# Performance work log

Measured on AMD Instinct MI355X. Metric: run time of the kernel, lower is better.

## Reference

```python
import jax, jax.numpy as jnp
import numpy as np

N_HEAD = 12


def setup_inputs() -> dict:
    key = jax.random.key(0)
    ks = jax.random.split(key, 16)
    B, N, D, P, H = 1, 512, 384, 128, N_HEAD
    s = 0.02
    return {
        'x1d': jax.random.normal(ks[0], (B, N, D), jnp.float32),
        'x2d': jax.random.normal(ks[1], (B, N, N, P), jnp.float32),
        'pose_t': jax.random.normal(ks[2], (B, N, 3), jnp.float32),
        'pose_r': jax.random.normal(ks[3], (B, N, 3, 3), jnp.float32),
        'bias': jnp.zeros((B, 1, N, N), jnp.float32),
        'w_sq': jax.random.normal(ks[4], (D, D), jnp.float32) * s,
        'w_sk': jax.random.normal(ks[5], (D, D), jnp.float32) * s,
        'w_sv': jax.random.normal(ks[6], (D, D), jnp.float32) * s,
        'w_pb': jax.random.normal(ks[7], (P, H), jnp.float32) * s,
        'w_pq': jax.random.normal(ks[8], (D, H * 3 * 4), jnp.float32) * s,
        'w_pk': jax.random.normal(ks[9], (D, H * 3 * 4), jnp.float32) * s,
        'w_pv': jax.random.normal(ks[10], (D, H * 3 * 8), jnp.float32) * s,
        'tpw': jax.random.uniform(ks[11], (H,), jnp.float32),
        'w_pairv': jax.random.normal(ks[12], (P, D), jnp.float32) * s,
        'w_out': jax.random.normal(ks[13], (2 * D + H * 8 * 4, D), jnp.float32) * s,
        'b_out': jnp.zeros((D,), jnp.float32),
    }


def reference(x1d, x2d, pose_t, pose_r, bias, w_sq, w_sk, w_sv, w_pb,
              w_pq, w_pk, w_pv, tpw, w_pairv, w_out, b_out):
    B, N, D = x1d.shape
    H = N_HEAD
    dk = D // H
    scalar_w = 1.0 / np.sqrt(3 * dk)
    point_w_c = 1.0 / np.sqrt(3 * 4 * 9 / 2)
    pair_w = 1.0 / np.sqrt(3)

    T = pose_t                                # [B,N,3]
    R = jnp.swapaxes(pose_r, -1, -2)          # [B,N,3,3] (pose[1]^T as in torch code)

    # scalar attention
    q_s = (x1d @ w_sq).reshape(B, N, H, dk)
    k_s = (x1d @ w_sk).reshape(B, N, H, dk)
    v_s = (x1d @ w_sv).reshape(B, N, H, dk)
    scalar_attn = jnp.einsum('bihc,bjhc->bhij', q_s * scalar_w, k_s)

    # point attention (global frame)
    def affine(pt):  # R @ pt + T
        return jnp.einsum('bnxy,bnhpy->bnhpx', R, pt) + T[:, :, None, None, :]

    q_p = affine((x1d @ w_pq).reshape(B, N, H, 4, 3))
    k_p = affine((x1d @ w_pk).reshape(B, N, H, 4, 3))
    v_p = affine((x1d @ w_pv).reshape(B, N, H, 8, 3))

    dist = jnp.linalg.norm(q_p[:, :, None] - k_p[:, None], axis=-1)  # [B,I,J,H,P]
    pw = point_w_c * jax.nn.softplus(tpw)                            # [H]
    point_attn = -0.5 * pw[:, None, None] * jnp.transpose(dist.sum(-1), (0, 3, 1, 2))

    # pair bias attention
    pair_attn = pair_w * jnp.transpose(x2d @ w_pb, (0, 3, 1, 2))     # [B,H,I,J]

    attn = jax.nn.softmax(scalar_attn + point_attn + pair_attn + bias, axis=-1)

    # aggregations
    out_scalar = jnp.einsum('bhij,bjhc->bihc', attn, v_s).reshape(B, N, D)

    out_pg = jnp.einsum('bhij,bjhcp->bihcp', attn, v_p)              # [B,I,H,8,3]
    # inverse affine: R^T @ (x - T)
    out_pl = jnp.einsum('bnyx,bnhpy->bnhpx', R, out_pg - T[:, :, None, None, :])
    out_pn = jnp.linalg.norm(out_pl, axis=-1).reshape(B, N, H * 8)
    out_pl = out_pl.reshape(B, N, H * 8 * 3)

    v_pair = (x2d @ w_pairv).reshape(B, N, N, H, dk)
    out_pair = jnp.einsum('bhij,bijhc->bihc', attn, v_pair).reshape(B, N, D)

    feat = jnp.concatenate([out_scalar, out_pl, out_pair, out_pn], axis=-1)
    return feat @ w_out + b_out
```

## Files before the change

### kernel.cpp

```cpp
#include <hip/hip_runtime.h>
#include <hip/hip_bf16.h>
#include <math.h>

#define N_  512
#define D_  384
#define H_  12
#define DK_ 32
#define P_  128

typedef short short8 __attribute__((ext_vector_type(8)));
typedef float f32x4  __attribute__((ext_vector_type(4)));

static __device__ __forceinline__ unsigned short f2bf(float f) {
    union { float f; unsigned int u; } v; v.f = f;
    unsigned int r = (v.u + 0x7FFFu + ((v.u >> 16) & 1u)) >> 16;
    return (unsigned short)r;
}
static __device__ __forceinline__ float bf2f(unsigned short u) {
    union { unsigned int u; float f; } v; v.u = ((unsigned int)u) << 16;
    return v.f;
}
static __device__ __forceinline__ short2 pk2bf(float a, float b) {
    __hip_bfloat162 h = __float22bfloat162_rn(make_float2(a, b));
    return *(short2*)&h;
}
typedef union { short8 v; short2 h2[4]; } s8u;

__global__ __launch_bounds__(384) void k_front(
    const float* __restrict__ x2d, const float* __restrict__ w_pb,
    float* __restrict__ pairlog,
    const float* __restrict__ x1d, const float* __restrict__ pose_t,
    const float* __restrict__ pose_r,
    const float* __restrict__ w_sq, const float* __restrict__ w_sk,
    const float* __restrict__ w_sv, const float* __restrict__ w_pq,
    const float* __restrict__ w_pk, const float* __restrict__ w_pv,
    float* __restrict__ qs, float* __restrict__ kst,
    float* __restrict__ qp, float* __restrict__ kpt,
    unsigned short* __restrict__ vcatT)
{
    __shared__ float raw[8][288];
    __shared__ float Rsh[8][9];
    __shared__ float Tsh[8][3];

    const int t = threadIdx.x;

    if (blockIdx.x < 2048) {
        if (t >= 256) return;
        const int wid  = t >> 6;
        const int lane = t & 63;
        const int quad = lane >> 4;
        const int col  = lane & 15;
        const float pair_w = 0.57735027f;

        short8 bfr[4];
        #pragma unroll
        for (int kt = 0; kt < 4; ++kt) {
            #pragma unroll
            for (int jj = 0; jj < 8; ++jj) {
                int p = kt * 32 + quad * 8 + jj;
                bfr[kt][jj] = (col < 12) ? (short)f2bf(w_pb[p * 12 + col]) : (short)0;
            }
        }
        #pragma unroll
        for (int s = 0; s < 2; ++s) {
            const int T  = blockIdx.x * 8 + wid * 2 + s;
            const int i  = T >> 5;
            const int j0 = (T & 31) << 4;
            const float* xrow = x2d + ((size_t)(i * N_) + j0 + col) * P_;

            f32x4 acc = {0.f, 0.f, 0.f, 0.f};
            #pragma unroll
            for (int kt = 0; kt < 4; ++kt) {
                const int k0 = kt * 32 + quad * 8;
                float4 f0 = *(const float4*)(xrow + k0);
                float4 f1 = *(const float4*)(xrow + k0 + 4);
                s8u afr;
                afr.h2[0] = pk2bf(f0.x, f0.y);
                afr.h2[1] = pk2bf(f0.z, f0.w);
                afr.h2[2] = pk2bf(f1.x, f1.y);
                afr.h2[3] = pk2bf(f1.z, f1.w);
                acc = __builtin_amdgcn_mfma_f32_16x16x32_bf16(afr.v, bfr[kt], acc, 0, 0, 0);
            }
            if (col < 12) {
                #pragma unroll
                for (int r = 0; r < 4; ++r) {
                    int j = j0 + quad * 4 + r;
                    pairlog[((size_t)(col * N_ + i)) * N_ + j] = pair_w * acc[r];
                }
            }
        }
        return;
    }

    const int b   = blockIdx.x - 2048;
    const int seg = b >> 6;
    const int i0  = (b & 63) * 8;

    if (seg < 3) {
        const float* __restrict__ w = (seg == 0) ? w_sq : (seg == 1) ? w_sk : w_sv;
        float acc[8];
        #pragma unroll
        for (int r = 0; r < 8; ++r) acc[r] = 0.f;
        for (int d = 0; d < D_; d += 4) {
            float4 xr[8];
            #pragma unroll
            for (int r = 0; r < 8; ++r)
                xr[r] = *(const float4*)(x1d + (i0 + r) * D_ + d);
            #pragma unroll
            for (int e = 0; e < 4; ++e) {
                float wv = w[(d + e) * D_ + t];
                #pragma unroll
                for (int r = 0; r < 8; ++r)
                    acc[r] += ((const float*)&xr[r])[e] * wv;
            }
        }
        if (seg == 0) {
            #pragma unroll
            for (int r = 0; r < 8; ++r) qs[(i0 + r) * D_ + t] = acc[r];
        } else if (seg == 1) {
            *(float4*)(kst + t * N_ + i0)     = make_float4(acc[0], acc[1], acc[2], acc[3]);
            *(float4*)(kst + t * N_ + i0 + 4) = make_float4(acc[4], acc[5], acc[6], acc[7]);
        } else {
            int h = t >> 5, c = t & 31;
            s8u sv;
            #pragma unroll
            for (int r = 0; r < 4; ++r) sv.h2[r] = pk2bf(acc[2*r], acc[2*r+1]);
            *(short8*)(vcatT + ((size_t)h * 64 + c) * N_ + i0) = sv.v;
        }
    } else {
        if (t < 72) Rsh[t / 9][t % 9] = pose_r[(i0 + t / 9) * 9 + t % 9];
        else if (t < 96) {
            int r = (t - 72) / 3, c = (t - 72) % 3;
            Tsh[r][c] = pose_t[(i0 + r) * 3 + c];
        }

        if (t < 288) {
            const float* __restrict__ w;
            int col, ldw;
            if (seg == 3) {
                if (t < 144) { w = w_pq; col = t;       ldw = 144; }
                else         { w = w_pk; col = t - 144; ldw = 144; }
            } else         { w = w_pv; col = t;       ldw = 288; }
            float acc[8];
            #pragma unroll
            for (int r = 0; r < 8; ++r) acc[r] = 0.f;
            for (int d = 0; d < D_; d += 4) {
                float4 xr[8];
                #pragma unroll
                for (int r = 0; r < 8; ++r)
                    xr[r] = *(const float4*)(x1d + (i0 + r) * D_ + d);
                #pragma unroll
                for (int e = 0; e < 4; ++e) {
                    float wv = w[(d + e) * ldw + col];
                    #pragma unroll
                    for (int r = 0; r < 8; ++r)
                        acc[r] += ((const float*)&xr[r])[e] * wv;
                }
            }
            #pragma unroll
            for (int r = 0; r < 8; ++r) raw[r][t] = acc[r];
        }
        __syncthreads();

        if (t < 288) {
            const int x3   = t % 3;
            const int base = t - x3;
            if (seg == 3) {
                const int c = (t < 144) ? t : t - 144;
                if (t < 144) {
                    #pragma unroll
                    for (int r = 0; r < 8; ++r) {
                        float g = Rsh[r][0 + x3] * raw[r][base]
                                + Rsh[r][3 + x3] * raw[r][base + 1]
                                + Rsh[r][6 + x3] * raw[r][base + 2] + Tsh[r][x3];
                        qp[(i0 + r) * 144 + c] = g;
                    }
                } else {
                    float g[8];
                    #pragma unroll
                    for (int r = 0; r < 8; ++r)
                        g[r] = Rsh[r][0 + x3] * raw[r][base]
                             + Rsh[r][3 + x3] * raw[r][base + 1]
                             + Rsh[r][6 + x3] * raw[r][base + 2] + Tsh[r][x3];
                    *(float4*)(kpt + c * N_ + i0)     = make_float4(g[0], g[1], g[2], g[3]);
                    *(float4*)(kpt + c * N_ + i0 + 4) = make_float4(g[4], g[5], g[6], g[7]);
                }
            } else {
                int h = t / 24, pc = t % 24;
                float g[8];
                #pragma unroll
                for (int r = 0; r < 8; ++r)
                    g[r] = Rsh[r][0 + x3] * raw[r][base]
                         + Rsh[r][3 + x3] * raw[r][base + 1]
                         + Rsh[r][6 + x3] * raw[r][base + 2] + Tsh[r][x3];
                s8u sv;
                #pragma unroll
                for (int r = 0; r < 4; ++r) sv.h2[r] = pk2bf(g[2*r], g[2*r+1]);
                *(short8*)(vcatT + ((size_t)h * 64 + 32 + pc) * N_ + i0) = sv.v;
            }
        }
    }
}

__global__ __launch_bounds__(256) void k_sp_soft(
    const float* __restrict__ qs, const float* __restrict__ kst,
    const float* __restrict__ qp, const float* __restrict__ kpt,
    const float* __restrict__ bias, const float* __restrict__ tpw,
    const float* __restrict__ pairlog,
    unsigned short* __restrict__ attn_bf)
{
    const int h  = blockIdx.x / 128;
    const int i0 = (blockIdx.x % 128) * 4;
    const int t  = threadIdx.x;
    const int lane = t & 63;
    const int wid  = t >> 6;
    __shared__ float qsh[4][32];
    __shared__ float qph[4][12];
    __shared__ float wredm[4][4];
    __shared__ float wreds[4][4];
    if (t < 128) { int il = t / 32, c = t % 32; qsh[il][c] = qs[(i0+il) * D_ + h*32 + c]; }
    else if (t < 176) { int r = t - 128; int il = r / 12, c = r % 12; qph[il][c] = qp[(i0+il)*144 + h*12 + c]; }
    const float pwh = 0.13608276f * log1pf(expf(tpw[h]));
    const float scalar_w = 0.10206207f;
    __syncthreads();

    float v[4][2];
    for (int jh = 0; jh < 2; ++jh) {
        int j = t + jh * 256;
        float kv[32];
        #pragma unroll
        for (int c = 0; c < 32; ++c) kv[c] = kst[(h*32 + c) * N_ + j];
        float kp[12];
        #pragma unroll
        for (int c = 0; c < 12; ++c) kp[c] = kpt[(h*12 + c) * N_ + j];

        #pragma unroll
        for (int il = 0; il < 4; ++il) {
            float s = 0.f;
            #pragma unroll
            for (int c = 0; c < 32; ++c) s += qsh[il][c] * kv[c];
            float dsum = 0.f;
            #pragma unroll
            for (int p = 0; p < 4; ++p) {
                float dx = qph[il][p*3+0] - kp[p*3+0];
                float dy = qph[il][p*3+1] - kp[p*3+1];
                float dz = qph[il][p*3+2] - kp[p*3+2];
                dsum += sqrtf(dx*dx + dy*dy + dz*dz);
            }
            v[il][jh] = scalar_w * s - 0.5f * pwh * dsum
                      + bias[(i0+il) * N_ + j]
                      + pairlog[((size_t)(h * N_ + (i0+il))) * N_ + j];
        }
    }

    #pragma unroll
    for (int il = 0; il < 4; ++il) {
        float mt = fmaxf(v[il][0], v[il][1]);
        #pragma unroll
        for (int off = 1; off < 64; off <<= 1)
            mt = fmaxf(mt, __shfl_xor(mt, off));
        if (lane == 0) wredm[il][wid] = mt;
    }
    __syncthreads();
    float m[4];
    #pragma unroll
    for (int il = 0; il < 4; ++il)
        m[il] = fmaxf(fmaxf(wredm[il][0], wredm[il][1]),
                      fmaxf(wredm[il][2], wredm[il][3]));

    #pragma unroll
    for (int il = 0; il < 4; ++il) {
        float e0 = __expf(v[il][0] - m[il]);
        float e1 = __expf(v[il][1] - m[il]);
        v[il][0] = e0; v[il][1] = e1;
        float st = e0 + e1;
        #pragma unroll
        for (int off = 1; off < 64; off <<= 1)
            st += __shfl_xor(st, off);
        if (lane == 0) wreds[il][wid] = st;
    }
    __syncthreads();
    #pragma unroll
    for (int il = 0; il < 4; ++il) {
        float inv = 1.0f / (wreds[il][0] + wreds[il][1] + wreds[il][2] + wreds[il][3]);
        size_t base = ((size_t)(h * N_ + i0 + il)) * N_;
        attn_bf[base + t]       = f2bf(v[il][0] * inv);
        attn_bf[base + t + 256] = f2bf(v[il][1] * inv);
    }
}

__global__ __launch_bounds__(256) void k_mid(
    const unsigned short* __restrict__ attn_bf,
    const float* __restrict__ x2d,
    const unsigned short* __restrict__ vcatT,
    float* __restrict__ tmp,
    float* __restrict__ feat, float* __restrict__ outpg)
{
    __shared__ float4 at[3][N_];
    __shared__ float red[4][1536];

    const int t = threadIdx.x;

    if (blockIdx.x < 512) {
        const int i = blockIdx.x;
        for (int idx = t; idx < 12 * N_; idx += 256) {
            int h = idx >> 9, j = idx & 511;
            float a = bf2f(attn_bf[((size_t)(h * N_ + i)) * N_ + j]);
            ((float*)&at[h >> 2][j])[h & 3] = a;
        }
        __syncthreads();

        const int p2 = (t & 63) * 2;
        const int jh = t >> 6;
        float acc[12][2];
        #pragma unroll
        for (int h = 0; h < 12; ++h) { acc[h][0] = 0.f; acc[h][1] = 0.f; }
        const float* xb = x2d + (size_t)i * N_ * P_;

        #pragma unroll 4
        for (int j = jh; j < N_; j += 4) {
            float2 x = *(const float2*)(xb + j * P_ + p2);
            float4 a0 = at[0][j], a1 = at[1][j], a2 = at[2][j];
            acc[0][0]  += a0.x*x.x; acc[0][1]  += a0.x*x.y;
            acc[1][0]  += a0.y*x.x; acc[1][1]  += a0.y*x.y;
            acc[2][0]  += a0.z*x.x; acc[2][1]  += a0.z*x.y;
            acc[3][0]  += a0.w*x.x; acc[3][1]  += a0.w*x.y;
            acc[4][0]  += a1.x*x.x; acc[4][1]  += a1.x*x.y;
            acc[5][0]  += a1.y*x.x; acc[5][1]  += a1.y*x.y;
            acc[6][0]  += a1.z*x.x; acc[6][1]  += a1.z*x.y;
            acc[7][0]  += a1.w*x.x; acc[7][1]  += a1.w*x.y;
            acc[8][0]  += a2.x*x.x; acc[8][1]  += a2.x*x.y;
            acc[9][0]  += a2.y*x.x; acc[9][1]  += a2.y*x.y;
            acc[10][0] += a2.z*x.x; acc[10][1] += a2.z*x.y;
            acc[11][0] += a2.w*x.x; acc[11][1] += a2.w*x.y;
        }
        #pragma unroll
        for (int h = 0; h < 12; ++h) {
            red[jh][h * 128 + p2]     = acc[h][0];
            red[jh][h * 128 + p2 + 1] = acc[h][1];
        }
        __syncthreads();
        for (int idx = t; idx < 1536; idx += 256)
            tmp[(size_t)i * 1536 + idx] = red[0][idx] + red[1][idx] + red[2][idx] + red[3][idx];
        return;
    }

    const int bid  = blockIdx.x - 512;
    const int h    = bid >> 5;
    const int i0   = (bid & 31) << 4;
    const int wid  = t >> 6;
    const int lane = t & 63;
    const int quad = lane >> 4;
    const int col  = lane & 15;
    const int c    = wid * 16 + col;
    const bool cvalid = (c < 56);

    const unsigned short* arow = attn_bf + ((size_t)(h * N_ + i0 + col)) * N_;
    const unsigned short* brow = vcatT + ((size_t)h * 64 + c) * N_;

    f32x4 acc = {0.f, 0.f, 0.f, 0.f};
    #pragma unroll
    for (int kt = 0; kt < 16; ++kt) {
        const int k0 = kt * 32 + quad * 8;
        short8 a = *(const short8*)(arow + k0);
        short8 b;
        if (cvalid) b = *(const short8*)(brow + k0);
        else { b[0]=0;b[1]=0;b[2]=0;b[3]=0;b[4]=0;b[5]=0;b[6]=0;b[7]=0; }
        acc = __builtin_amdgcn_mfma_f32_16x16x32_bf16(a, b, acc, 0, 0, 0);
    }
    #pragma unroll
    for (int r = 0; r < 4; ++r) {
        int i = i0 + quad * 4 + r;
        if (c < 32)       feat[(size_t)i * 1152 + h * 32 + c] = acc[r];
        else if (c < 56)  outpg[((size_t)i * 12 + h) * 24 + (c - 32)] = acc[r];
    }
}

__global__ __launch_bounds__(384) void k_feat(
    const float* __restrict__ tmp, const float* __restrict__ outpg,
    const float* __restrict__ pose_t, const float* __restrict__ pose_r,
    const float* __restrict__ w_pairv, float* __restrict__ feat)
{
    const int i = blockIdx.x;
    const int t = threadIdx.x;
    __shared__ float tsh[1536];
    __shared__ float pg[288];
    __shared__ float pl[288];
    __shared__ float Rsh[9], Tsh[3];

    for (int idx = t; idx < 1536; idx += 384) tsh[idx] = tmp[(size_t)i * 1536 + idx];
    if (t < 288) pg[t] = outpg[i * 288 + t];
    if (t < 9) Rsh[t] = pose_r[i * 9 + t];
    if (t < 3) Tsh[t] = pose_t[i * 3 + t];
    __syncthreads();

    {
        int h = t >> 5;
        const float* ts = tsh + h * 128;
        float acc = 0.f;
        #pragma unroll 4
        for (int p = 0; p < 128; ++p) acc += ts[p] * w_pairv[p * D_ + t];
        feat[(size_t)i * 1152 + 672 + t] = acc;
    }
    if (t < 288) {
        int x3 = t % 3, base = t - x3;
        float g0 = pg[base + 0] - Tsh[0];
        float g1 = pg[base + 1] - Tsh[1];
        float g2 = pg[base + 2] - Tsh[2];
        float v = Rsh[x3*3+0]*g0 + Rsh[x3*3+1]*g1 + Rsh[x3*3+2]*g2;
        pl[t] = v;
        feat[(size_t)i * 1152 + 384 + t] = v;
    }
    __syncthreads();
    if (t < 96) {
        float a = pl[t*3], b = pl[t*3+1], c = pl[t*3+2];
        feat[(size_t)i * 1152 + 1056 + t] = sqrtf(a*a + b*b + c*c);
    }
}

__global__ __launch_bounds__(384) void k_out_part(
    const float* __restrict__ feat, const float* __restrict__ w_out,
    float* __restrict__ part)
{
    const int kc = blockIdx.x >> 6;
    const int i0 = (blockIdx.x & 63) * 8;
    const int t  = threadIdx.x;
    const int k0 = kc * 144;

    float acc[8];
    #pragma unroll
    for (int r = 0; r < 8; ++r) acc[r] = 0.f;

    for (int d = 0; d < 144; d += 4) {
        float4 fr[8];
        #pragma unroll
        for (int r = 0; r < 8; ++r)
            fr[r] = *(const float4*)(feat + (size_t)(i0 + r) * 1152 + k0 + d);
        #pragma unroll
        for (int e = 0; e < 4; ++e) {
            float wv = w_out[(size_t)(k0 + d + e) * D_ + t];
            #pragma unroll
            for (int r = 0; r < 8; ++r)
                acc[r] += ((const float*)&fr[r])[e] * wv;
        }
    }
    #pragma unroll
    for (int r = 0; r < 8; ++r)
        part[((size_t)kc * N_ + i0 + r) * D_ + t] = acc[r];
}

__global__ __launch_bounds__(256) void k_out_red(
    const float* __restrict__ part, const float* __restrict__ b_out,
    float* __restrict__ out)
{
    const int idx = blockIdx.x * 256 + threadIdx.x;
    float s = b_out[idx % D_];
    #pragma unroll
    for (int kc = 0; kc < 8; ++kc) s += part[(size_t)kc * (N_ * D_) + idx];
    out[idx] = s;
}

extern "C" void kernel_launch(void* const* d_in, const int* in_sizes, int n_in,
                              void* d_out, int out_size, void* d_ws, size_t ws_size,
                              hipStream_t stream)
{
    (void)in_sizes; (void)n_in; (void)out_size; (void)ws_size;
    const float* x1d     = (const float*)d_in[0];
    const float* x2d     = (const float*)d_in[1];
    const float* pose_t  = (const float*)d_in[2];
    const float* pose_r  = (const float*)d_in[3];
    const float* bias    = (const float*)d_in[4];
    const float* w_sq    = (const float*)d_in[5];
    const float* w_sk    = (const float*)d_in[6];
    const float* w_sv    = (const float*)d_in[7];
    const float* w_pb    = (const float*)d_in[8];
    const float* w_pq    = (const float*)d_in[9];
    const float* w_pk    = (const float*)d_in[10];
    const float* w_pv    = (const float*)d_in[11];
    const float* tpw     = (const float*)d_in[12];
    const float* w_pairv = (const float*)d_in[13];
    const float* w_out   = (const float*)d_in[14];
    const float* b_out   = (const float*)d_in[15];
    float* out = (float*)d_out;

    float* ws = (float*)d_ws;
    float* qs      = ws;
    float* kst     = qs      + 196608;
    float* qp      = kst     + 196608;
    float* kpt     = qp      + 73728;
    float* pairlog = kpt     + 73728;
    float* tmp     = pairlog + 3145728;
    float* outpg   = tmp     + 786432;
    float* feat    = outpg   + 147456;
    float* part    = feat    + 589824;
    unsigned short* attn_bf = (unsigned short*)(part + 1572864);
    unsigned short* vcatT   = attn_bf + (size_t)12 * N_ * N_;

    hipLaunchKernelGGL(k_front, dim3(2048 + 320), dim3(384), 0, stream,
                       x2d, w_pb, pairlog,
                       x1d, pose_t, pose_r, w_sq, w_sk, w_sv, w_pq, w_pk, w_pv,
                       qs, kst, qp, kpt, vcatT);
    hipLaunchKernelGGL(k_sp_soft, dim3(12 * 128), dim3(256), 0, stream,
                       qs, kst, qp, kpt, bias, tpw, pairlog, attn_bf);
    hipLaunchKernelGGL(k_mid, dim3(512 + 384), dim3(256), 0, stream,
                       attn_bf, x2d, vcatT, tmp, feat, outpg);
    hipLaunchKernelGGL(k_feat, dim3(N_), dim3(384), 0, stream,
                       tmp, outpg, pose_t, pose_r, w_pairv, feat);
    hipLaunchKernelGGL(k_out_part, dim3(512), dim3(384), 0, stream,
                       feat, w_out, part);
    hipLaunchKernelGGL(k_out_red, dim3(768), dim3(256), 0, stream,
                       part, b_out, out);
}
```

Baseline: 361.3 us.

## Use all warps for pair-bias tiles, hoist x2d loads, halve projection rows per block

The pair-bias part of k_front now uses all six waves per block instead of four, so fewer blocks are needed. All x2d loads are issued ahead of the MFMA work behind a sched_barrier to raise memory-level parallelism, and the pairlog stores become float4 writes. The projection blocks now handle 4 rows instead of 8, doubling their block count to spread the small GEMMs across more CUs. The cost is more registers held for the prefetched tiles and extra redundant weight reads in the projection blocks.

Result: slower. 368.9 us (+2.1%).

```diff
diff --git a/kernel.cpp b/kernel.cpp
--- a/kernel.cpp
+++ b/kernel.cpp
@@ -8,6 +8,8 @@
 #define DK_ 32
 #define P_  128
 
+#define NPB 1366
+
 typedef short short8 __attribute__((ext_vector_type(8)));
 typedef float f32x4  __attribute__((ext_vector_type(4)));
 
@@ -25,6 +27,7 @@
     return *(short2*)&h;
 }
 typedef union { short8 v; short2 h2[4]; } s8u;
+typedef union { short2 h2[2]; unsigned long long u; } s4u;
 
 __global__ __launch_bounds__(384) void k_front(
     const float* __restrict__ x2d, const float* __restrict__ w_pb,
@@ -38,14 +41,13 @@
     float* __restrict__ qp, float* __restrict__ kpt,
     unsigned short* __restrict__ vcatT)
 {
-    __shared__ float raw[8][288];
-    __shared__ float Rsh[8][9];
-    __shared__ float Tsh[8][3];
+    __shared__ float raw[4][288];
+    __shared__ float Rsh[4][9];
+    __shared__ float Tsh[4][3];
 
     const int t = threadIdx.x;
 
-    if (blockIdx.x < 2048) {
-        if (t >= 256) return;
+    if (blockIdx.x < NPB) {
         const int wid  = t >> 6;
         const int lane = t & 63;
         const int quad = lane >> 4;
@@ -61,76 +63,91 @@
                 bfr[kt][jj] = (col < 12) ? (short)f2bf(w_pb[p * 12 + col]) : (short)0;
             }
         }
+
+        const int Tb = blockIdx.x * 12 + wid * 2;
+
+        float4 f[2][8];
+        int iA[2], j0A[2];
         #pragma unroll
         for (int s = 0; s < 2; ++s) {
-            const int T  = blockIdx.x * 8 + wid * 2 + s;
-            const int i  = T >> 5;
-            const int j0 = (T & 31) << 4;
-            const float* xrow = x2d + ((size_t)(i * N_) + j0 + col) * P_;
-
-            f32x4 acc = {0.f, 0.f, 0.f, 0.f};
-            #pragma unroll
-            for (int kt = 0; kt < 4; ++kt) {
-                const int k0 = kt * 32 + quad * 8;
-                float4 f0 = *(const float4*)(xrow + k0);
-                float4 f1 = *(const float4*)(xrow + k0 + 4);
-                s8u afr;
-                afr.h2[0] = pk2bf(f0.x, f0.y);
-                afr.h2[1] = pk2bf(f0.z, f0.w);
-                afr.h2[2] = pk2bf(f1.x, f1.y);
-                afr.h2[3] = pk2bf(f1.z, f1.w);
-                acc = __builtin_amdgcn_mfma_f32_16x16x32_bf16(afr.v, bfr[kt], acc, 0, 0, 0);
-            }
-            if (col < 12) {
-                #pragma unroll
-                for (int r = 0; r < 4; ++r) {
-                    int j = j0 + quad * 4 + r;
-                    pairlog[((size_t)(col * N_ + i)) * N_ + j] = pair_w * acc[r];
+            const int T = Tb + s;
+            iA[s]  = T >> 5;
+            j0A[s] = (T & 31) << 4;
+            if (T < 16384) {
+                const float* xrow = x2d + ((size_t)(iA[s] * N_) + j0A[s] + col) * P_;
+                #pragma unroll
+                for (int kt = 0; kt < 4; ++kt) {
+                    f[s][2*kt]   = *(const float4*)(xrow + kt * 32 + quad * 8);
+                    f[s][2*kt+1] = *(const float4*)(xrow + kt * 32 + quad * 8 + 4);
                 }
             }
         }
+        __builtin_amdgcn_sched_barrier(0);
+
+        #pragma unroll
+        for (int s = 0; s < 2; ++s) {
+            const int T = Tb + s;
+            if (T < 16384) {
+                f32x4 acc = {0.f, 0.f, 0.f, 0.f};
+                #pragma unroll
+                for (int kt = 0; kt < 4; ++kt) {
+                    s8u afr;
+                    afr.h2[0] = pk2bf(f[s][2*kt].x,   f[s][2*kt].y);
+                    afr.h2[1] = pk2bf(f[s][2*kt].z,   f[s][2*kt].w);
+                    afr.h2[2] = pk2bf(f[s][2*kt+1].x, f[s][2*kt+1].y);
+                    afr.h2[3] = pk2bf(f[s][2*kt+1].z, f[s][2*kt+1].w);
+                    acc = __builtin_amdgcn_mfma_f32_16x16x32_bf16(afr.v, bfr[kt], acc, 0, 0, 0);
+                }
+                if (col < 12) {
+                    float4 st = make_float4(pair_w * acc[0], pair_w * acc[1],
+                                            pair_w * acc[2], pair_w * acc[3]);
+                    *(float4*)(pairlog + ((size_t)(col * N_ + iA[s])) * N_
+                               + j0A[s] + quad * 4) = st;
+                }
+            }
+        }
         return;
     }
 
-    const int b   = blockIdx.x - 2048;
-    const int seg = b >> 6;
-    const int i0  = (b & 63) * 8;
+    const int b   = blockIdx.x - NPB;
+    const int seg = b >> 7;
+    const int i0  = (b & 127) * 4;
 
     if (seg < 3) {
         const float* __restrict__ w = (seg == 0) ? w_sq : (seg == 1) ? w_sk : w_sv;
-        float acc[8];
-        #pragma unroll
-        for (int r = 0; r < 8; ++r) acc[r] = 0.f;
+        float acc[4];
+        #pragma unroll
+        for (int r = 0; r < 4; ++r) acc[r] = 0.f;
+        #pragma unroll 2
         for (int d = 0; d < D_; d += 4) {
-            float4 xr[8];
-            #pragma unroll
-            for (int r = 0; r < 8; ++r)
+            float4 xr[4];
+            #pragma unroll
+            for (int r = 0; r < 4; ++r)
                 xr[r] = *(const float4*)(x1d + (i0 + r) * D_ + d);
             #pragma unroll
             for (int e = 0; e < 4; ++e) {
                 float wv = w[(d + e) * D_ + t];
                 #pragma unroll
-                for (int r = 0; r < 8; ++r)
+                for (int r = 0; r < 4; ++r)
                     acc[r] += ((const float*)&xr[r])[e] * wv;
             }
         }
         if (seg == 0) {
             #pragma unroll
-            for (int r = 0; r < 8; ++r) qs[(i0 + r) * D_ + t] = acc[r];
+            for (int r = 0; r < 4; ++r) qs[(i0 + r) * D_ + t] = acc[r];
         } else if (seg == 1) {
-            *(float4*)(kst + t * N_ + i0)     = make_float4(acc[0], acc[1], acc[2], acc[3]);
-            *(float4*)(kst + t * N_ + i0 + 4) = make_float4(acc[4], acc[5], acc[6], acc[7]);
+            *(float4*)(kst + t * N_ + i0) = make_float4(acc[0], acc[1], acc[2], acc[3]);
         } else {
             int h = t >> 5, c = t & 31;
-            s8u sv;
-            #pragma unroll
-            for (int r = 0; r < 4; ++r) sv.h2[r] = pk2bf(acc[2*r], acc[2*r+1]);
-            *(short8*)(vcatT + ((size_t)h * 64 + c) * N_ + i0) = sv.v;
+            s4u sv;
+            sv.h2[0] = pk2bf(acc[0], acc[1]);
+            sv.h2[1] = pk2bf(acc[2], acc[3]);
+            *(unsigned long long*)(vcatT + ((size_t)h * 64 + c) * N_ + i0) = sv.u;
         }
     } else {
-        if (t < 72) Rsh[t / 9][t % 9] = pose_r[(i0 + t / 9) * 9 + t % 9];
-        else if (t < 96) {
-            int r = (t - 72) / 3, c = (t - 72) % 3;
+        if (t < 36) Rsh[t / 9][t % 9] = pose_r[(i0 + t / 9) * 9 + t % 9];
+        else if (t < 48) {
+            int r = (t - 36) / 3, c = (t - 36) % 3;
             Tsh[r][c] = pose_t[(i0 + r) * 3 + c];
         }
 
@@ -141,24 +158,25 @@
                 if (t < 144) { w = w_pq; col = t;       ldw = 144; }
                 else         { w = w_pk; col = t - 144; ldw = 144; }
             } else         { w = w_pv; col = t;       ldw = 288; }
-            float acc[8];
-            #pragma unroll
-            for (int r = 0; r < 8; ++r) acc[r] = 0.f;
+            float acc[4];
+            #pragma unroll
+            for (int r = 0; r < 4; ++r) acc[r] = 0.f;
+            #pragma unroll 2
             for (int d = 0; d < D_; d += 4) {
-                float4 xr[8];
-                #pragma unroll
-                for (int r = 0; r < 8; ++r)
+                float4 xr[4];
+                #pragma unroll
+                for (int r = 0; r < 4; ++r)
                     xr[r] = *(const float4*)(x1d + (i0 + r) * D_ + d);
                 #pragma unroll
                 for (int e = 0; e < 4; ++e) {
                     float wv = w[(d + e) * ldw + col];
                     #pragma unroll
-                    for (int r = 0; r < 8; ++r)
+                    for (int r = 0; r < 4; ++r)
                         acc[r] += ((const float*)&xr[r])[e] * wv;
                 }
             }
             #pragma unroll
-            for (int r = 0; r < 8; ++r) raw[r][t] = acc[r];
+            for (int r = 0; r < 4; ++r) raw[r][t] = acc[r];
         }
         __syncthreads();
 
@@ -167,36 +185,31 @@
             const int base = t - x3;
             if (seg == 3) {
                 const int c = (t < 144) ? t : t - 144;
+                float g[4];
+                #pragma unroll
+                for (int r = 0; r < 4; ++r)
+                    g[r] = Rsh[r][0 + x3] * raw[r][base]
+                         + Rsh[r][3 + x3] * raw[r][base + 1]
+                         + Rsh[r][6 + x3] * raw[r][base + 2] + Tsh[r][x3];
                 if (t < 144) {
                     #pragma unroll
-                    for (int r = 0; r < 8; ++r) {
-                        float g = Rsh[r][0 + x3] * raw[r][base]
-                                + Rsh[r][3 + x3] * raw[r][base + 1]
-                                + Rsh[r][6 + x3] * raw[r][base + 2] + Tsh[r][x3];
-                        qp[(i0 + r) * 144 + c] = g;
-                    }
+                    for (int r = 0; r < 4; ++r)
+                        qp[(i0 + r) * 144 + c] = g[r];
                 } else {
-                    float g[8];
-                    #pragma unroll
-                    for (int r = 0; r < 8; ++r)
-                        g[r] = Rsh[r][0 + x3] * raw[r][base]
-                             + Rsh[r][3 + x3] * raw[r][base + 1]
-                             + Rsh[r][6 + x3] * raw[r][base + 2] + Tsh[r][x3];
-                    *(float4*)(kpt + c * N_ + i0)     = make_float4(g[0], g[1], g[2], g[3]);
-                    *(float4*)(kpt + c * N_ + i0 + 4) = make_float4(g[4], g[5], g[6], g[7]);
+                    *(float4*)(kpt + c * N_ + i0) = make_float4(g[0], g[1], g[2], g[3]);
                 }
             } else {
                 int h = t / 24, pc = t % 24;
-                float g[8];
-                #pragma unroll
-                for (int r = 0; r < 8; ++r)
+                float g[4];
+                #pragma unroll
+                for (int r = 0; r < 4; ++r)
                     g[r] = Rsh[r][0 + x3] * raw[r][base]
                          + Rsh[r][3 + x3] * raw[r][base + 1]
                          + Rsh[r][6 + x3] * raw[r][base + 2] + Tsh[r][x3];
-                s8u sv;
-                #pragma unroll
-                for (int r = 0; r < 4; ++r) sv.h2[r] = pk2bf(g[2*r], g[2*r+1]);
-                *(short8*)(vcatT + ((size_t)h * 64 + 32 + pc) * N_ + i0) = sv.v;
+                s4u sv;
+                sv.h2[0] = pk2bf(g[0], g[1]);
+                sv.h2[1] = pk2bf(g[2], g[3]);
+                *(unsigned long long*)(vcatT + ((size_t)h * 64 + 32 + pc) * N_ + i0) = sv.u;
             }
         }
     }
@@ -496,7 +509,7 @@
     unsigned short* attn_bf = (unsigned short*)(part + 1572864);
     unsigned short* vcatT   = attn_bf + (size_t)12 * N_ * N_;
 
-    hipLaunchKernelGGL(k_front, dim3(2048 + 320), dim3(384), 0, stream,
+    hipLaunchKernelGGL(k_front, dim3(NPB + 640), dim3(384), 0, stream,
                        x2d, w_pb, pairlog,
                        x1d, pose_t, pose_r, w_sq, w_sk, w_sv, w_pq, w_pk, w_pv,
                        qs, kst, qp, kpt, vcatT);
```

## Persist pair-bias blocks with double-buffered loads and halve grids of later kernels

Applied to the files above, without the earlier changes.

The pair-bias projection in k_front becomes a persistent-style loop. 512 blocks of 6 waves each process strided tiles, double-buffering the x2d loads so the next tile's loads overlap the current MFMA, and stores use float4. Projection blocks are moved to the front of the grid. The other kernels (softmax, feat, out_part, out_red) each process 2–3 virtual blocks per physical block with smaller grids, which amortizes setup but reduces parallelism and adds extra syncs.

Measured after the change: 388.1 us. 7.4% more time.

```diff
diff --git a/kernel.cpp b/kernel.cpp
--- a/kernel.cpp
+++ b/kernel.cpp
@@ -7,6 +7,9 @@
 #define H_  12
 #define DK_ 32
 #define P_  128
+
+#define PROJ_B 320
+#define PAIR_B 512
 
 typedef short short8 __attribute__((ext_vector_type(8)));
 typedef float f32x4  __attribute__((ext_vector_type(4)));
@@ -44,12 +47,13 @@
 
     const int t = threadIdx.x;
 
-    if (blockIdx.x < 2048) {
-        if (t >= 256) return;
+    if (blockIdx.x >= PROJ_B) {
+        const int pb   = blockIdx.x - PROJ_B;
         const int wid  = t >> 6;
         const int lane = t & 63;
         const int quad = lane >> 4;
         const int col  = lane & 15;
+        const int gw   = pb * 6 + wid;
         const float pair_w = 0.57735027f;
 
         short8 bfr[4];
@@ -61,38 +65,51 @@
                 bfr[kt][jj] = (col < 12) ? (short)f2bf(w_pb[p * 12 + col]) : (short)0;
             }
         }
-        #pragma unroll
-        for (int s = 0; s < 2; ++s) {
-            const int T  = blockIdx.x * 8 + wid * 2 + s;
+
+        auto ldt = [&](float4* f, int T) {
             const int i  = T >> 5;
             const int j0 = (T & 31) << 4;
             const float* xrow = x2d + ((size_t)(i * N_) + j0 + col) * P_;
-
+            #pragma unroll
+            for (int kt = 0; kt < 4; ++kt) {
+                f[2*kt]   = *(const float4*)(xrow + kt * 32 + quad * 8);
+                f[2*kt+1] = *(const float4*)(xrow + kt * 32 + quad * 8 + 4);
+            }
+        };
+        auto cmpt = [&](const float4* f, int T) {
             f32x4 acc = {0.f, 0.f, 0.f, 0.f};
             #pragma unroll
             for (int kt = 0; kt < 4; ++kt) {
-                const int k0 = kt * 32 + quad * 8;
-                float4 f0 = *(const float4*)(xrow + k0);
-                float4 f1 = *(const float4*)(xrow + k0 + 4);
                 s8u afr;
-                afr.h2[0] = pk2bf(f0.x, f0.y);
-                afr.h2[1] = pk2bf(f0.z, f0.w);
-                afr.h2[2] = pk2bf(f1.x, f1.y);
-                afr.h2[3] = pk2bf(f1.z, f1.w);
+                afr.h2[0] = pk2bf(f[2*kt].x,   f[2*kt].y);
+                afr.h2[1] = pk2bf(f[2*kt].z,   f[2*kt].w);
+                afr.h2[2] = pk2bf(f[2*kt+1].x, f[2*kt+1].y);
+                afr.h2[3] = pk2bf(f[2*kt+1].z, f[2*kt+1].w);
                 acc = __builtin_amdgcn_mfma_f32_16x16x32_bf16(afr.v, bfr[kt], acc, 0, 0, 0);
             }
             if (col < 12) {
-                #pragma unroll
-                for (int r = 0; r < 4; ++r) {
-                    int j = j0 + quad * 4 + r;
-                    pairlog[((size_t)(col * N_ + i)) * N_ + j] = pair_w * acc[r];
-                }
-            }
-        }
+                const int i  = T >> 5;
+                const int j0 = (T & 31) << 4;
+                float4 st = make_float4(pair_w * acc[0], pair_w * acc[1],
+                                        pair_w * acc[2], pair_w * acc[3]);
+                *(float4*)(pairlog + ((size_t)(col * N_ + i)) * N_ + j0 + quad * 4) = st;
+            }
+        };
+
+        float4 fA[8], fB[8];
+        const bool has6 = (gw + 15360) < 16384;
+        ldt(fA, gw);
+        ldt(fB, gw + 3072);
+        cmpt(fA, gw);          ldt(fA, gw + 6144);
+        cmpt(fB, gw + 3072);   ldt(fB, gw + 9216);
+        cmpt(fA, gw + 6144);   ldt(fA, gw + 12288);
+        cmpt(fB, gw + 9216);   if (has6) ldt(fB, gw + 15360);
+        cmpt(fA, gw + 12288);
+        if (has6) cmpt(fB, gw + 15360);
         return;
     }
 
-    const int b   = blockIdx.x - 2048;
+    const int b   = blockIdx.x;
     const int seg = b >> 6;
     const int i0  = (b & 63) * 8;
 
@@ -209,83 +226,89 @@
     const float* __restrict__ pairlog,
     unsigned short* __restrict__ attn_bf)
 {
-    const int h  = blockIdx.x / 128;
-    const int i0 = (blockIdx.x % 128) * 4;
-    const int t  = threadIdx.x;
+    const int t = threadIdx.x;
     const int lane = t & 63;
     const int wid  = t >> 6;
     __shared__ float qsh[4][32];
     __shared__ float qph[4][12];
     __shared__ float wredm[4][4];
     __shared__ float wreds[4][4];
-    if (t < 128) { int il = t / 32, c = t % 32; qsh[il][c] = qs[(i0+il) * D_ + h*32 + c]; }
-    else if (t < 176) { int r = t - 128; int il = r / 12, c = r % 12; qph[il][c] = qp[(i0+il)*144 + h*12 + c]; }
-    const float pwh = 0.13608276f * log1pf(expf(tpw[h]));
-    const float scalar_w = 0.10206207f;
-    __syncthreads();
-
-    float v[4][2];
-    for (int jh = 0; jh < 2; ++jh) {
-        int j = t + jh * 256;
-        float kv[32];
-        #pragma unroll
-        for (int c = 0; c < 32; ++c) kv[c] = kst[(h*32 + c) * N_ + j];
-        float kp[12];
-        #pragma unroll
-        for (int c = 0; c < 12; ++c) kp[c] = kpt[(h*12 + c) * N_ + j];
+
+    for (int u = 0; u < 2; ++u) {
+        const int vb = blockIdx.x + u * 768;
+        const int h  = vb / 128;
+        const int i0 = (vb % 128) * 4;
+
+        if (t < 128) { int il = t / 32, c = t % 32; qsh[il][c] = qs[(i0+il) * D_ + h*32 + c]; }
+        else if (t < 176) { int r = t - 128; int il = r / 12, c = r % 12; qph[il][c] = qp[(i0+il)*144 + h*12 + c]; }
+        const float pwh = 0.13608276f * log1pf(expf(tpw[h]));
+        const float scalar_w = 0.10206207f;
+        __syncthreads();
+
+        float v[4][2];
+        for (int jh = 0; jh < 2; ++jh) {
+            int j = t + jh * 256;
+            float kv[32];
+            #pragma unroll
+            for (int c = 0; c < 32; ++c) kv[c] = kst[(h*32 + c) * N_ + j];
+            float kp[12];
+            #pragma unroll
+            for (int c = 0; c < 12; ++c) kp[c] = kpt[(h*12 + c) * N_ + j];
+
+            #pragma unroll
+            for (int il = 0; il < 4; ++il) {
+                float s = 0.f;
+                #pragma unroll
+                for (int c = 0; c < 32; ++c) s += qsh[il][c] * kv[c];
+                float dsum = 0.f;
+                #pragma unroll
+                for (int p = 0; p < 4; ++p) {
+                    float dx = qph[il][p*3+0] - kp[p*3+0];
+                    float dy = qph[il][p*3+1] - kp[p*3+1];
+                    float dz = qph[il][p*3+2] - kp[p*3+2];
+                    dsum += sqrtf(dx*dx + dy*dy + dz*dz);
+                }
+                v[il][jh] = scalar_w * s - 0.5f * pwh * dsum
+                          + bias[(i0+il) * N_ + j]
+                          + pairlog[((size_t)(h * N_ + (i0+il))) * N_ + j];
+            }
+        }
 
         #pragma unroll
         for (int il = 0; il < 4; ++il) {
-            float s = 0.f;
-            #pragma unroll
-            for (int c = 0; c < 32; ++c) s += qsh[il][c] * kv[c];
-            float dsum = 0.f;
-            #pragma unroll
-            for (int p = 0; p < 4; ++p) {
-                float dx = qph[il][p*3+0] - kp[p*3+0];
-                float dy = qph[il][p*3+1] - kp[p*3+1];
-                float dz = qph[il][p*3+2] - kp[p*3+2];
-                dsum += sqrtf(dx*dx + dy*dy + dz*dz);
-            }
-            v[il][jh] = scalar_w * s - 0.5f * pwh * dsum
-                      + bias[(i0+il) * N_ + j]
-                      + pairlog[((size_t)(h * N_ + (i0+il))) * N_ + j];
-        }
-    }
-
-    #pragma unroll
-    for (int il = 0; il < 4; ++il) {
-        float mt = fmaxf(v[il][0], v[il][1]);
-        #pragma unroll
-        for (int off = 1; off < 64; off <<= 1)
-            mt = fmaxf(mt, __shfl_xor(mt, off));
-        if (lane == 0) wredm[il][wid] = mt;
-    }
-    __syncthreads();
-    float m[4];
-    #pragma unroll
-    for (int il = 0; il < 4; ++il)
-        m[il] = fmaxf(fmaxf(wredm[il][0], wredm[il][1]),
-                      fmaxf(wredm[il][2], wredm[il][3]));
-
-    #pragma unroll
-    for (int il = 0; il < 4; ++il) {
-        float e0 = __expf(v[il][0] - m[il]);
-        float e1 = __expf(v[il][1] - m[il]);
-        v[il][0] = e0; v[il][1] = e1;
-        float st = e0 + e1;
-        #pragma unroll
-        for (int off = 1; off < 64; off <<= 1)
-            st += __shfl_xor(st, off);
-        if (lane == 0) wreds[il][wid] = st;
-    }
-    __syncthreads();
-    #pragma unroll
-    for (int il = 0; il < 4; ++il) {
-        float inv = 1.0f / (wreds[il][0] + wreds[il][1] + wreds[il][2] + wreds[il][3]);
-        size_t base = ((size_t)(h * N_ + i0 + il)) * N_;
-        attn_bf[base + t]       = f2bf(v[il][0] * inv);
-        attn_bf[base + t + 256] = f2bf(v[il][1] * inv);
+            float mt = fmaxf(v[il][0], v[il][1]);
+            #pragma unroll
+            for (int off = 1; off < 64; off <<= 1)
+                mt = fmaxf(mt, __shfl_xor(mt, off));
+            if (lane == 0) wredm[il][wid] = mt;
+        }
+        __syncthreads();
+        float m[4];
+        #pragma unroll
+        for (int il = 0; il < 4; ++il)
+            m[il] = fmaxf(fmaxf(wredm[il][0], wredm[il][1]),
+                          fmaxf(wredm[il][2], wredm[il][3]));
+
+        #pragma unroll
+        for (int il = 0; il < 4; ++il) {
+            float e0 = __expf(v[il][0] - m[il]);
+            float e1 = __expf(v[il][1] - m[il]);
+            v[il][0] = e0; v[il][1] = e1;
+            float st = e0 + e1;
+            #pragma unroll
+            for (int off = 1; off < 64; off <<= 1)
+                st += __shfl_xor(st, off);
+            if (lane == 0) wreds[il][wid] = st;
+        }
+        __syncthreads();
+        #pragma unroll
+        for (int il = 0; il < 4; ++il) {
+            float inv = 1.0f / (wreds[il][0] + wreds[il][1] + wreds[il][2] + wreds[il][3]);
+            size_t base = ((size_t)(h * N_ + i0 + il)) * N_;
+            attn_bf[base + t]       = f2bf(v[il][0] * inv);
+            attn_bf[base + t + 256] = f2bf(v[il][1] * inv);
+        }
+        __syncthreads();
     }
 }
 
@@ -381,40 +404,44 @@
     const float* __restrict__ pose_t, const float* __restrict__ pose_r,
     const float* __restrict__ w_pairv, float* __restrict__ feat)
 {
-    const int i = blockIdx.x;
     const int t = threadIdx.x;
     __shared__ float tsh[1536];
     __shared__ float pg[288];
     __shared__ float pl[288];
     __shared__ float Rsh[9], Tsh[3];
 
-    for (int idx = t; idx < 1536; idx += 384) tsh[idx] = tmp[(size_t)i * 1536 + idx];
-    if (t < 288) pg[t] = outpg[i * 288 + t];
-    if (t < 9) Rsh[t] = pose_r[i * 9 + t];
-    if (t < 3) Tsh[t] = pose_t[i * 3 + t];
-    __syncthreads();
-
-    {
-        int h = t >> 5;
-        const float* ts = tsh + h * 128;
-        float acc = 0.f;
-        #pragma unroll 4
-        for (int p = 0; p < 128; ++p) acc += ts[p] * w_pairv[p * D_ + t];
-        feat[(size_t)i * 1152 + 672 + t] = acc;
-    }
-    if (t < 288) {
-        int x3 = t % 3, base = t - x3;
-        float g0 = pg[base + 0] - Tsh[0];
-        float g1 = pg[base + 1] - Tsh[1];
-        float g2 = pg[base + 2] - Tsh[2];
-        float v = Rsh[x3*3+0]*g0 + Rsh[x3*3+1]*g1 + Rsh[x3*3+2]*g2;
-        pl[t] = v;
-        feat[(size_t)i * 1152 + 384 + t] = v;
-    }
-    __syncthreads();
-    if (t < 96) {
-        float a = pl[t*3], b = pl[t*3+1], c = pl[t*3+2];
-        feat[(size_t)i * 1152 + 1056 + t] = sqrtf(a*a + b*b + c*c);
+    for (int u = 0; u < 2; ++u) {
+        const int i = blockIdx.x + u * 256;
+
+        for (int idx = t; idx < 1536; idx += 384) tsh[idx] = tmp[(size_t)i * 1536 + idx];
+        if (t < 288) pg[t] = outpg[i * 288 + t];
+        if (t < 9) Rsh[t] = pose_r[i * 9 + t];
+        if (t < 3) Tsh[t] = pose_t[i * 3 + t];
+        __syncthreads();
+
+        {
+            int h = t >> 5;
+            const float* ts = tsh + h * 128;
+            float acc = 0.f;
+            #pragma unroll 4
+            for (int p = 0; p < 128; ++p) acc += ts[p] * w_pairv[p * D_ + t];
+            feat[(size_t)i * 1152 + 672 + t] = acc;
+        }
+        if (t < 288) {
+            int x3 = t % 3, base = t - x3;
+            float g0 = pg[base + 0] - Tsh[0];
+            float g1 = pg[base + 1] - Tsh[1];
+            float g2 = pg[base + 2] - Tsh[2];
+            float v = Rsh[x3*3+0]*g0 + Rsh[x3*3+1]*g1 + Rsh[x3*3+2]*g2;
+            pl[t] = v;
+            feat[(size_t)i * 1152 + 384 + t] = v;
+        }
+        __syncthreads();
+        if (t < 96) {
+            float a = pl[t*3], b = pl[t*3+1], c = pl[t*3+2];
+            feat[(size_t)i * 1152 + 1056 + t] = sqrtf(a*a + b*b + c*c);
+        }
+        __syncthreads();
     }
 }
 
@@ -422,42 +449,49 @@
     const float* __restrict__ feat, const float* __restrict__ w_out,
     float* __restrict__ part)
 {
-    const int kc = blockIdx.x >> 6;
-    const int i0 = (blockIdx.x & 63) * 8;
-    const int t  = threadIdx.x;
-    const int k0 = kc * 144;
-
-    float acc[8];
-    #pragma unroll
-    for (int r = 0; r < 8; ++r) acc[r] = 0.f;
-
-    for (int d = 0; d < 144; d += 4) {
-        float4 fr[8];
+    const int t = threadIdx.x;
+    for (int u = 0; u < 2; ++u) {
+        const int vb = blockIdx.x + u * 256;
+        const int kc = vb >> 6;
+        const int i0 = (vb & 63) * 8;
+        const int k0 = kc * 144;
+
+        float acc[8];
+        #pragma unroll
+        for (int r = 0; r < 8; ++r) acc[r] = 0.f;
+
+        for (int d = 0; d < 144; d += 4) {
+            float4 fr[8];
+            #pragma unroll
+            for (int r = 0; r < 8; ++r)
+                fr[r] = *(const float4*)(feat + (size_t)(i0 + r) * 1152 + k0 + d);
+            #pragma unroll
+            for (int e = 0; e < 4; ++e) {
+                float wv = w_out[(size_t)(k0 + d + e) * D_ + t];
+                #pragma unroll
+                for (int r = 0; r < 8; ++r)
+                    acc[r] += ((const float*)&fr[r])[e] * wv;
+            }
+        }
         #pragma unroll
         for (int r = 0; r < 8; ++r)
-            fr[r] = *(const float4*)(feat + (size_t)(i0 + r) * 1152 + k0 + d);
-        #pragma unroll
-        for (int e = 0; e < 4; ++e) {
-            float wv = w_out[(size_t)(k0 + d + e) * D_ + t];
-            #pragma unroll
-            for (int r = 0; r < 8; ++r)
-                acc[r] += ((const float*)&fr[r])[e] * wv;
-        }
-    }
-    #pragma unroll
-    for (int r = 0; r < 8; ++r)
-        part[((size_t)kc * N_ + i0 + r) * D_ + t] = acc[r];
+            part[((size_t)kc * N_ + i0 + r) * D_ + t] = acc[r];
+    }
 }
 
 __global__ __launch_bounds__(256) void k_out_red(
     const float* __restrict__ part, const float* __restrict__ b_out,
     float* __restrict__ out)
 {
-    const int idx = blockIdx.x * 256 + threadIdx.x;
-    float s = b_out[idx % D_];
+    const int t = threadIdx.x;
     #pragma unroll
-    for (int kc = 0; kc < 8; ++kc) s += part[(size_t)kc * (N_ * D_) + idx];
-    out[idx] = s;
+    for (int u = 0; u < 3; ++u) {
+        const int idx = blockIdx.x * 256 + t + u * 65536;
+        float s = b_out[idx % D_];
+        #pragma unroll
+        for (int kc = 0; kc < 8; ++kc) s += part[(size_t)kc * (N_ * D_) + idx];
+        out[idx] = s;
+    }
 }
 
 extern "C" void kernel_launch(void* const* d_in, const int* in_sizes, int n_in,
@@ -496,18 +530,18 @@
     unsigned short* attn_bf = (unsigned short*)(part + 1572864);
     unsigned short* vcatT   = attn_bf + (size_t)12 * N_ * N_;
 
-    hipLaunchKernelGGL(k_front, dim3(2048 + 320), dim3(384), 0, stream,
+    hipLaunchKernelGGL(k_front, dim3(PROJ_B + PAIR_B), dim3(384), 0, stream,
                        x2d, w_pb, pairlog,
                        x1d, pose_t, pose_r, w_sq, w_sk, w_sv, w_pq, w_pk, w_pv,
                        qs, kst, qp, kpt, vcatT);
-    hipLaunchKernelGGL(k_sp_soft, dim3(12 * 128), dim3(256), 0, stream,
+    hipLaunchKernelGGL(k_sp_soft, dim3(768), dim3(256), 0, stream,
                        qs, kst, qp, kpt, bias, tpw, pairlog, attn_bf);
     hipLaunchKernelGGL(k_mid, dim3(512 + 384), dim3(256), 0, stream,
                        attn_bf, x2d, vcatT, tmp, feat, outpg);
-    hipLaunchKernelGGL(k_feat, dim3(N_), dim3(384), 0, stream,
+    hipLaunchKernelGGL(k_feat, dim3(256), dim3(384), 0, stream,
                        tmp, outpg, pose_t, pose_r, w_pairv, feat);
-    hipLaunchKernelGGL(k_out_part, dim3(512), dim3(384), 0, stream,
+    hipLaunchKernelGGL(k_out_part, dim3(256), dim3(384), 0, stream,
                        feat, w_out, part);
-    hipLaunchKernelGGL(k_out_red, dim3(768), dim3(256), 0, stream,
+    hipLaunchKernelGGL(k_out_red, dim3(256), dim3(256), 0, stream,
                        part, b_out, out);
 }
```

## Make pair-bias projection persistent with coalesced loads, LDS staging and prefetch

Applied to the files above, without the earlier changes.

The pair-bias part of k_front becomes a persistent loop: 512 blocks of 6 waves, each wave handling up to 6 tiles, instead of 2048 blocks of 4 waves doing 2 tiles each. Each tile is read from x2d with fully coalesced float4 loads, staged through a swizzled LDS buffer to form the MFMA operands, and the next tiles' loads are issued in registers before the current tile is computed. The pairlog store becomes a single float4 per lane, and projection blocks are reordered to launch first. This targets the bandwidth-bound read of x2d, at the cost of higher register use (launch_bounds 384,3) and 48KB of shared memory per block, which may reduce occupancy.

Result: slower. 407.6 us (+12.8%).

```diff
diff --git a/kernel.cpp b/kernel.cpp
--- a/kernel.cpp
+++ b/kernel.cpp
@@ -8,6 +8,9 @@
 #define DK_ 32
 #define P_  128
 
+#define PROJ_B 320
+#define PAIR_B 512
+
 typedef short short8 __attribute__((ext_vector_type(8)));
 typedef float f32x4  __attribute__((ext_vector_type(4)));
 
@@ -26,7 +29,7 @@
 }
 typedef union { short8 v; short2 h2[4]; } s8u;
 
-__global__ __launch_bounds__(384) void k_front(
+__global__ __launch_bounds__(384, 3) void k_front(
     const float* __restrict__ x2d, const float* __restrict__ w_pb,
     float* __restrict__ pairlog,
     const float* __restrict__ x1d, const float* __restrict__ pose_t,
@@ -38,19 +41,20 @@
     float* __restrict__ qp, float* __restrict__ kpt,
     unsigned short* __restrict__ vcatT)
 {
-    __shared__ float raw[8][288];
-    __shared__ float Rsh[8][9];
-    __shared__ float Tsh[8][3];
+    __shared__ float smem[12288];
 
     const int t = threadIdx.x;
 
-    if (blockIdx.x < 2048) {
-        if (t >= 256) return;
+    if (blockIdx.x >= PROJ_B) {
+        const int pb   = blockIdx.x - PROJ_B;
         const int wid  = t >> 6;
         const int lane = t & 63;
         const int quad = lane >> 4;
         const int col  = lane & 15;
+        const int gw   = pb * 6 + wid;
         const float pair_w = 0.57735027f;
+
+        float* wl = smem + wid * 2048;
 
         short8 bfr[4];
         #pragma unroll
@@ -61,38 +65,62 @@
                 bfr[kt][jj] = (col < 12) ? (short)f2bf(w_pb[p * 12 + col]) : (short)0;
             }
         }
-        #pragma unroll
-        for (int s = 0; s < 2; ++s) {
-            const int T  = blockIdx.x * 8 + wid * 2 + s;
-            const int i  = T >> 5;
-            const int j0 = (T & 31) << 4;
-            const float* xrow = x2d + ((size_t)(i * N_) + j0 + col) * P_;
-
+
+        auto LDT = [&](float4* f, int T) {
+            const float* tb = x2d + ((size_t)((T >> 5) * N_ + ((T & 31) << 4))) * P_;
+            #pragma unroll
+            for (int k = 0; k < 8; ++k)
+                f[k] = *(const float4*)(tb + k * 256 + lane * 4);
+        };
+        auto CMP = [&](const float4* f, int T, bool dostore) {
+            #pragma unroll
+            for (int k = 0; k < 8; ++k) {
+                int off  = k * 1024 + lane * 16;
+                int soff = off ^ (((off >> 9) & 7) << 4);
+                *(float4*)((char*)wl + soff) = f[k];
+            }
             f32x4 acc = {0.f, 0.f, 0.f, 0.f};
             #pragma unroll
             for (int kt = 0; kt < 4; ++kt) {
-                const int k0 = kt * 32 + quad * 8;
-                float4 f0 = *(const float4*)(xrow + k0);
-                float4 f1 = *(const float4*)(xrow + k0 + 4);
+                int g0 = (col * 512 + kt * 128 + quad * 32) ^ ((col & 7) << 4);
+                float4 x0 = *(const float4*)((const char*)wl + g0);
+                float4 x1 = *(const float4*)((const char*)wl + (g0 ^ 16));
                 s8u afr;
-                afr.h2[0] = pk2bf(f0.x, f0.y);
-                afr.h2[1] = pk2bf(f0.z, f0.w);
-                afr.h2[2] = pk2bf(f1.x, f1.y);
-                afr.h2[3] = pk2bf(f1.z, f1.w);
+                afr.h2[0] = pk2bf(x0.x, x0.y);
+                afr.h2[1] = pk2bf(x0.z, x0.w);
+                afr.h2[2] = pk2bf(x1.x, x1.y);
+                afr.h2[3] = pk2bf(x1.z, x1.w);
                 acc = __builtin_amdgcn_mfma_f32_16x16x32_bf16(afr.v, bfr[kt], acc, 0, 0, 0);
             }
-            if (col < 12) {
-                #pragma unroll
-                for (int r = 0; r < 4; ++r) {
-                    int j = j0 + quad * 4 + r;
-                    pairlog[((size_t)(col * N_ + i)) * N_ + j] = pair_w * acc[r];
-                }
-            }
-        }
+            if (dostore && col < 12) {
+                const int i  = T >> 5;
+                const int j0 = (T & 31) << 4;
+                float4 st = make_float4(pair_w * acc[0], pair_w * acc[1],
+                                        pair_w * acc[2], pair_w * acc[3]);
+                *(float4*)(pairlog + ((size_t)(col * N_ + i)) * N_ + j0 + quad * 4) = st;
+            }
+        };
+
+        const bool has6 = (gw + 15360) < 16384;
+        const int  T5   = has6 ? (gw + 15360) : gw;
+
+        float4 fA[8], fB[8], fC[8];
+        LDT(fA, gw);
+        LDT(fB, gw + 3072);
+        LDT(fC, gw + 6144);   CMP(fA, gw,          true);
+        LDT(fA, gw + 9216);   CMP(fB, gw + 3072,   true);
+        LDT(fB, gw + 12288);  CMP(fC, gw + 6144,   true);
+        LDT(fC, T5);          CMP(fA, gw + 9216,   true);
+        CMP(fB, gw + 12288, true);
+        CMP(fC, T5, has6);
         return;
     }
 
-    const int b   = blockIdx.x - 2048;
+    float (*raw)[288] = reinterpret_cast<float(*)[288]>(smem);
+    float (*Rsh)[9]   = reinterpret_cast<float(*)[9]>(smem + 2304);
+    float (*Tsh)[3]   = reinterpret_cast<float(*)[3]>(smem + 2304 + 72);
+
+    const int b   = blockIdx.x;
     const int seg = b >> 6;
     const int i0  = (b & 63) * 8;
 
@@ -496,7 +524,7 @@
     unsigned short* attn_bf = (unsigned short*)(part + 1572864);
     unsigned short* vcatT   = attn_bf + (size_t)12 * N_ * N_;
 
-    hipLaunchKernelGGL(k_front, dim3(2048 + 320), dim3(384), 0, stream,
+    hipLaunchKernelGGL(k_front, dim3(PROJ_B + PAIR_B), dim3(384), 0, stream,
                        x2d, w_pb, pairlog,
                        x1d, pose_t, pose_r, w_sq, w_sk, w_sv, w_pq, w_pk, w_pv,
                        qs, kst, qp, kpt, vcatT);
```
